# Performance work log

Hardware: AMD Instinct MI355X
Metric: run time of the kernel (lower is better)

The kernel has to match this reference:

```python
import jax, jax.numpy as jnp
import numpy as np

B, N, D = 32, 2048, 16
PCD = 2        # point_cloud_dimensions
K_NN = 16      # k nearest neighbours
FILTERS = 64


def setup_inputs() -> dict:
    key = jax.random.key(0)
    k1, k2, k3 = jax.random.split(key, 3)
    x = jax.random.normal(k1, (B, N, D), dtype=jnp.float32)
    # 1x1 Conv2D == dense over the last (channel) dim: W [D, FILTERS], b [FILTERS]
    W = jax.random.normal(k2, (D, FILTERS), dtype=jnp.float32) * (1.0 / np.sqrt(D))
    b = jnp.zeros((FILTERS,), dtype=jnp.float32)
    return {"x": x, "W": W, "b": b}


def reference(x, W, b):
    # points = first PCD channels; features = full input (dynamic_coordinates=True)
    points = x[:, :, :PCD]                                   # [B,N,PCD]
    # squared pairwise distances: ||p_i||^2 + ||p_j||^2 - 2 p_i.p_j  -> [B,N,N]
    sq = jnp.sum(points * points, axis=-1)                   # [B,N]
    dist = sq[:, :, None] + sq[:, None, :] - 2.0 * jnp.einsum(
        'bnd,bmd->bnm', points, points)
    # k nearest neighbours (smallest distance) per point -> [B,N,k]
    _, idx = jax.lax.top_k(-dist, K_NN)
    # gather neighbour features: [B,N,k,D]
    neigh = jax.vmap(lambda f, i: f[i])(x, idx)
    centre = x[:, :, None, :]                                # [B,N,1,D]
    # NOTE: source concatenates along the neighbour axis -> [B,N,k+1,D]
    edges = jnp.concatenate([centre, neigh - centre], axis=2)
    # 1x1 conv (linear activation) over channel dim: [B,N,k+1,FILTERS]
    conv = jnp.einsum('bnkd,df->bnkf', edges, W) + b
    # Max pooling over neighbour axis: [B,N,FILTERS]
    pooled = jnp.max(conv, axis=2)
    # shortcut_input_features=True: concat original features
    return jnp.concatenate([pooled, x], axis=-1)             # [B,N,FILTERS+D]
```

## Files before the change

### kernel.cpp

```cpp
#include <hip/hip_runtime.h>


#define B_  32
#define N_  2048
#define D_  16
#define F_  64
#define K_  16
#define OUTD (F_ + D_)
#define NQ  64
#define NS  4
#define SPLIT (N_ / NS)
#define CAP 24

typedef _Float16 h2 __attribute__((ext_vector_type(2)));

static __device__ __forceinline__ h2 h2min(h2 a, h2 b) { return __builtin_elementwise_min(a, b); }
static __device__ __forceinline__ h2 h2max(h2 a, h2 b) { return __builtin_elementwise_max(a, b); }
static __device__ __forceinline__ _Float16 hmn(_Float16 a, _Float16 b) { return __builtin_elementwise_min(a, b); }
static __device__ __forceinline__ _Float16 hmx(_Float16 a, _Float16 b) { return __builtin_elementwise_max(a, b); }
static __device__ __forceinline__ unsigned short h2b(_Float16 h) { return __builtin_bit_cast(unsigned short, h); }
static __device__ __forceinline__ _Float16 b2h(unsigned short b) { return __builtin_bit_cast(_Float16, b); }

static __device__ __forceinline__ void pair_ins(_Float16 (&k)[16], _Float16 y0, _Float16 y1) {
#pragma unroll
    for (int j = 15; j >= 2; --j)
        k[j] = hmn(hmn(k[j], hmx(k[j - 1], y0)), hmx(k[j - 2], y1));
    k[1] = hmn(hmn(k[1], hmx(k[0], y0)), y1);
    k[0] = hmn(k[0], y0);
}

static __device__ __forceinline__ float vdist(float2 qp, float sqn, float2 p, float sm) {
    float dot = __fmaf_rn(qp.y, p.y, __fmul_rn(qp.x, p.x));
    return __fsub_rn(__fadd_rn(sqn, sm), __fmul_rn(2.f, dot));
}

__global__ __launch_bounds__(256) void proj_kernel(const float* __restrict__ x,
                                                   const float* __restrict__ W,
                                                   float* __restrict__ Y) {
    __shared__ float Ws[D_ * F_];
    __shared__ float xs[16][D_];
    const int t = threadIdx.x;
    for (int i = t; i < D_ * F_; i += 256) Ws[i] = W[i];
    const int p0 = blockIdx.x * 16;
    ((float*)xs)[t] = x[(size_t)p0 * D_ + t];
    __syncthreads();
    const int w = t >> 6, f = t & 63;
#pragma unroll
    for (int i = 0; i < 4; i++) {
        const int pw = w * 4 + i;
        float acc = 0.f;
#pragma unroll
        for (int d = 0; d < D_; d++) acc = fmaf(xs[pw][d], Ws[d * F_ + f], acc);
        Y[(size_t)(p0 + pw) * F_ + f] = acc;
    }
}

__global__ __launch_bounds__(256, 4) void knn_kernel(const float* __restrict__ x,
                                                     const float* __restrict__ bias,
                                                     const float* __restrict__ Y,
                                                     float* __restrict__ out) {
    __shared__ float2 pts[N_];
    __shared__ float  sqs[N_];
    __shared__ __align__(16) char region[NS * NQ * CAP * 2];
    __shared__ unsigned short idxL[NQ][18];
    __shared__ int   scnt[NS][NQ];
    __shared__ float TubA[NQ];

    unsigned (*arr32)[NQ][9] = (unsigned (*)[NQ][9])region;
    unsigned short (*survb)[NQ][CAP] = (unsigned short (*)[NQ][CAP])region;

    const int b = blockIdx.x >> 5;
    const int qbase = (blockIdx.x & 31) * NQ;
    const int t = threadIdx.x;
    const int s = t >> 6;
    const int qi = t & 63;
    const int q = qbase + qi;

    const float* xb = x + (size_t)b * N_ * D_;
    for (int m = t; m < N_; m += 256) {
        float2 p = make_float2(xb[m * D_ + 0], xb[m * D_ + 1]);
        pts[m] = p;
        sqs[m] = __fadd_rn(__fmul_rn(p.x, p.x), __fmul_rn(p.y, p.y));
    }
    __syncthreads();

    const float2 qp = pts[q];
    const float sqn = sqs[q];
    const float n2x = -2.0f * qp.x, n2y = -2.0f * qp.y;

    h2 key2[16];
    const _Float16 hinf = b2h((unsigned short)0x7C00);
#pragma unroll
    for (int j = 0; j < 16; ++j) key2[j] = (h2){hinf, hinf};

    const int m0 = s * SPLIT, m1 = m0 + SPLIT;
#pragma unroll 4
    for (int m = m0; m < m1; m += 2) {
        float2 pa = pts[m];     float sa = sqs[m];
        float2 pb = pts[m + 1]; float sb = sqs[m + 1];
        float da = __fmaf_rn(n2y, pa.y, __fmaf_rn(n2x, pa.x, sqn + sa));
        float db = __fmaf_rn(n2y, pb.y, __fmaf_rn(n2x, pb.x, sqn + sb));
        h2 v = __builtin_bit_cast(h2, __builtin_amdgcn_cvt_pkrtz(da, db));
#pragma unroll
        for (int j = 15; j >= 1; --j)
            key2[j] = h2min(key2[j], h2max(key2[j - 1], v));
        key2[0] = h2min(key2[0], v);
    }

    _Float16 keyl[16];
#pragma unroll
    for (int j = 0; j < 16; ++j) keyl[j] = key2[j].x;
#pragma unroll
    for (int tt = 0; tt < 8; ++tt) pair_ins(keyl, key2[2 * tt].y, key2[2 * tt + 1].y);

    if (s > 0) {
#pragma unroll
        for (int tt = 0; tt < 8; ++tt)
            arr32[s - 1][qi][tt] =
                (unsigned)h2b(keyl[2 * tt]) | ((unsigned)h2b(keyl[2 * tt + 1]) << 16);
    }
    __syncthreads();

    if (s == 0) {
        for (int ss = 0; ss < NS - 1; ++ss) {
#pragma unroll
            for (int tt = 0; tt < 8; ++tt) {
                unsigned w32 = arr32[ss][qi][tt];
                pair_ins(keyl, b2h((unsigned short)(w32 & 0xffffu)),
                               b2h((unsigned short)(w32 >> 16)));
            }
        }
        float tub = (float)b2h((unsigned short)(h2b(keyl[15]) + 2));
        TubA[qi] = fmaxf(tub, 7e-5f);
    }
    __syncthreads();

    const float Tub = TubA[qi];
    int sc = 0;
#pragma unroll 2
    for (int m = m0; m < m1; ++m) {
        float d = vdist(qp, sqn, pts[m], sqs[m]);
        if (d < Tub) { if (sc < CAP) survb[s][qi][sc] = (unsigned short)m; sc++; }
    }
    scnt[s][qi] = sc;
    __syncthreads();

    if (s == 0) {
        float key[16];
#pragma unroll
        for (int j = 0; j < 16; ++j) key[j] = INFINITY;
        for (int ss = 0; ss < NS; ++ss) {
            int n = scnt[ss][qi]; n = n < CAP ? n : CAP;
            for (int j = 0; j < n; ++j) {
                int m = (int)survb[ss][qi][j];
                float d = vdist(qp, sqn, pts[m], sqs[m]);
#pragma unroll
                for (int jj = 15; jj >= 1; --jj)
                    key[jj] = fminf(key[jj], fmaxf(key[jj - 1], d));
                key[0] = fminf(key[0], d);
            }
        }
        const float T = key[15];
        int w = 0;
        for (int ss = 0; ss < NS; ++ss) {
            int n = scnt[ss][qi]; n = n < CAP ? n : CAP;
            for (int j = 0; j < n; ++j) {
                int m = (int)survb[ss][qi][j];
                float d = vdist(qp, sqn, pts[m], sqs[m]);
                if (d < T && w < K_) idxL[qi][w++] = (unsigned short)m;
            }
        }
        for (int ss = 0; ss < NS && w < K_; ++ss) {
            int n = scnt[ss][qi]; n = n < CAP ? n : CAP;
            for (int j = 0; j < n && w < K_; ++j) {
                int m = (int)survb[ss][qi][j];
                float d = vdist(qp, sqn, pts[m], sqs[m]);
                if (d == T) idxL[qi][w++] = (unsigned short)m;
            }
        }
    }
    __syncthreads();

    const int f = qi;
    const float bf = bias[f];
    const float* Yb = Y + (size_t)b * N_ * F_;
    for (int i = 0; i < 16; i++) {
        const int qq = s * 16 + i;
        const int gq = qbase + qq;
        const float yn = Yb[(size_t)gq * F_ + f];
        float M = -INFINITY;
#pragma unroll
        for (int k = 0; k < K_; k++) {
            int m = (int)idxL[qq][k];
            M = fmaxf(M, Yb[(size_t)m * F_ + f]);
        }
        const size_t pb = (size_t)b * N_ + gq;
        out[pb * OUTD + f] = fmaxf(yn, M - yn) + bf;
        if (f < D_) out[pb * OUTD + F_ + f] = xb[(size_t)gq * D_ + f];
    }
}

extern "C" void kernel_launch(void* const* d_in, const int* in_sizes, int n_in,
                              void* d_out, int out_size, void* d_ws, size_t ws_size,
                              hipStream_t stream) {
    const float* x    = (const float*)d_in[0];
    const float* W    = (const float*)d_in[1];
    const float* bias = (const float*)d_in[2];
    float* out = (float*)d_out;

    float* Y = (float*)d_ws;

    proj_kernel<<<B_ * N_ / 16, 256, 0, stream>>>(x, W, Y);
    knn_kernel <<<B_ * (N_ / NQ), 256, 0, stream>>>(x, bias, Y, out);
}
```

Baseline: 251.9 us.

## Process 128 queries per 512-thread kNN block to amortize point staging

Each kNN block now handles 128 queries with 512 threads (two groups of four split waves) instead of 64 queries with 256 threads. This halves the number of blocks that load the batch's 2048 points and squared norms into shared memory, so that staging cost is shared across more queries. It also clamps the survivor count when it is stored and pads any unfilled neighbour slots with the query itself, guarding against uninitialized indices. The larger block uses more shared memory and threads, which may lower occupancy, and the grid shrinks to 512 blocks.

New measurement: 259.8 us. +3.1%, slower.

```diff
diff --git a/kernel.cpp b/kernel.cpp
--- a/kernel.cpp
+++ b/kernel.cpp
@@ -7,7 +7,7 @@
 #define F_  64
 #define K_  16
 #define OUTD (F_ + D_)
-#define NQ  64
+#define NQB 128
 #define NS  4
 #define SPLIT (N_ / NS)
 #define CAP 24
@@ -27,11 +27,6 @@
         k[j] = hmn(hmn(k[j], hmx(k[j - 1], y0)), hmx(k[j - 2], y1));
     k[1] = hmn(hmn(k[1], hmx(k[0], y0)), y1);
     k[0] = hmn(k[0], y0);
-}
-
-static __device__ __forceinline__ float vdist(float2 qp, float sqn, float2 p, float sm) {
-    float dot = __fmaf_rn(qp.y, p.y, __fmul_rn(qp.x, p.x));
-    return __fsub_rn(__fadd_rn(sqn, sm), __fmul_rn(2.f, dot));
 }
 
 __global__ __launch_bounds__(256) void proj_kernel(const float* __restrict__ x,
@@ -55,29 +50,32 @@
     }
 }
 
-__global__ __launch_bounds__(256, 4) void knn_kernel(const float* __restrict__ x,
+__global__ __launch_bounds__(512, 2) void knn_kernel(const float* __restrict__ x,
                                                      const float* __restrict__ bias,
                                                      const float* __restrict__ Y,
                                                      float* __restrict__ out) {
     __shared__ float2 pts[N_];
     __shared__ float  sqs[N_];
-    __shared__ __align__(16) char region[NS * NQ * CAP * 2];
-    __shared__ unsigned short idxL[NQ][18];
-    __shared__ int   scnt[NS][NQ];
-    __shared__ float TubA[NQ];
-
-    unsigned (*arr32)[NQ][9] = (unsigned (*)[NQ][9])region;
-    unsigned short (*survb)[NQ][CAP] = (unsigned short (*)[NQ][CAP])region;
-
-    const int b = blockIdx.x >> 5;
-    const int qbase = (blockIdx.x & 31) * NQ;
+    __shared__ __align__(16) char region[NS * NQB * CAP * 2];
+    __shared__ unsigned short idxL[NQB][18];
+    __shared__ int   scnt[NS][NQB];
+    __shared__ float TubA[NQB];
+
+    unsigned (*arr32)[NQB][9] = (unsigned (*)[NQB][9])region;
+    unsigned short (*survb)[NQB][CAP] = (unsigned short (*)[NQB][CAP])region;
+
+    const int b = blockIdx.x >> 4;
+    const int qbase = (blockIdx.x & 15) * NQB;
     const int t = threadIdx.x;
-    const int s = t >> 6;
+    const int w8 = t >> 6;
+    const int s  = w8 & 3;
+    const int sg = w8 >> 2;
     const int qi = t & 63;
-    const int q = qbase + qi;
+    const int qloc = sg * 64 + qi;
+    const int q = qbase + qloc;
 
     const float* xb = x + (size_t)b * N_ * D_;
-    for (int m = t; m < N_; m += 256) {
+    for (int m = t; m < N_; m += 512) {
         float2 p = make_float2(xb[m * D_ + 0], xb[m * D_ + 1]);
         pts[m] = p;
         sqs[m] = __fadd_rn(__fmul_rn(p.x, p.x), __fmul_rn(p.y, p.y));
@@ -116,7 +114,7 @@
     if (s > 0) {
 #pragma unroll
         for (int tt = 0; tt < 8; ++tt)
-            arr32[s - 1][qi][tt] =
+            arr32[s - 1][qloc][tt] =
                 (unsigned)h2b(keyl[2 * tt]) | ((unsigned)h2b(keyl[2 * tt + 1]) << 16);
     }
     __syncthreads();
@@ -125,24 +123,26 @@
         for (int ss = 0; ss < NS - 1; ++ss) {
 #pragma unroll
             for (int tt = 0; tt < 8; ++tt) {
-                unsigned w32 = arr32[ss][qi][tt];
+                unsigned w32 = arr32[ss][qloc][tt];
                 pair_ins(keyl, b2h((unsigned short)(w32 & 0xffffu)),
                                b2h((unsigned short)(w32 >> 16)));
             }
         }
         float tub = (float)b2h((unsigned short)(h2b(keyl[15]) + 2));
-        TubA[qi] = fmaxf(tub, 7e-5f);
-    }
-    __syncthreads();
-
-    const float Tub = TubA[qi];
+        TubA[qloc] = fmaxf(tub, 7e-5f);
+    }
+    __syncthreads();
+
+    const float Tub = TubA[qloc];
     int sc = 0;
 #pragma unroll 2
     for (int m = m0; m < m1; ++m) {
-        float d = vdist(qp, sqn, pts[m], sqs[m]);
-        if (d < Tub) { if (sc < CAP) survb[s][qi][sc] = (unsigned short)m; sc++; }
-    }
-    scnt[s][qi] = sc;
+        float2 p = pts[m];
+        float dot = __fmaf_rn(qp.y, p.y, __fmul_rn(qp.x, p.x));
+        float d   = __fsub_rn(__fadd_rn(sqn, sqs[m]), __fmul_rn(2.f, dot));
+        if (d < Tub) { if (sc < CAP) survb[s][qloc][sc] = (unsigned short)m; sc++; }
+    }
+    scnt[s][qloc] = (sc < CAP) ? sc : CAP;
     __syncthreads();
 
     if (s == 0) {
@@ -150,10 +150,12 @@
 #pragma unroll
         for (int j = 0; j < 16; ++j) key[j] = INFINITY;
         for (int ss = 0; ss < NS; ++ss) {
-            int n = scnt[ss][qi]; n = n < CAP ? n : CAP;
+            int n = scnt[ss][qloc];
             for (int j = 0; j < n; ++j) {
-                int m = (int)survb[ss][qi][j];
-                float d = vdist(qp, sqn, pts[m], sqs[m]);
+                int m = (int)survb[ss][qloc][j];
+                float2 p = pts[m];
+                float dot = __fmaf_rn(qp.y, p.y, __fmul_rn(qp.x, p.x));
+                float d   = __fsub_rn(__fadd_rn(sqn, sqs[m]), __fmul_rn(2.f, dot));
 #pragma unroll
                 for (int jj = 15; jj >= 1; --jj)
                     key[jj] = fminf(key[jj], fmaxf(key[jj - 1], d));
@@ -163,21 +165,26 @@
         const float T = key[15];
         int w = 0;
         for (int ss = 0; ss < NS; ++ss) {
-            int n = scnt[ss][qi]; n = n < CAP ? n : CAP;
+            int n = scnt[ss][qloc];
             for (int j = 0; j < n; ++j) {
-                int m = (int)survb[ss][qi][j];
-                float d = vdist(qp, sqn, pts[m], sqs[m]);
-                if (d < T && w < K_) idxL[qi][w++] = (unsigned short)m;
+                int m = (int)survb[ss][qloc][j];
+                float2 p = pts[m];
+                float dot = __fmaf_rn(qp.y, p.y, __fmul_rn(qp.x, p.x));
+                float d   = __fsub_rn(__fadd_rn(sqn, sqs[m]), __fmul_rn(2.f, dot));
+                if (d < T && w < K_) idxL[qloc][w++] = (unsigned short)m;
             }
         }
         for (int ss = 0; ss < NS && w < K_; ++ss) {
-            int n = scnt[ss][qi]; n = n < CAP ? n : CAP;
+            int n = scnt[ss][qloc];
             for (int j = 0; j < n && w < K_; ++j) {
-                int m = (int)survb[ss][qi][j];
-                float d = vdist(qp, sqn, pts[m], sqs[m]);
-                if (d == T) idxL[qi][w++] = (unsigned short)m;
-            }
-        }
+                int m = (int)survb[ss][qloc][j];
+                float2 p = pts[m];
+                float dot = __fmaf_rn(qp.y, p.y, __fmul_rn(qp.x, p.x));
+                float d   = __fsub_rn(__fadd_rn(sqn, sqs[m]), __fmul_rn(2.f, dot));
+                if (d == T) idxL[qloc][w++] = (unsigned short)m;
+            }
+        }
+        while (w < K_) idxL[qloc][w++] = (unsigned short)q;
     }
     __syncthreads();
 
@@ -185,7 +192,7 @@
     const float bf = bias[f];
     const float* Yb = Y + (size_t)b * N_ * F_;
     for (int i = 0; i < 16; i++) {
-        const int qq = s * 16 + i;
+        const int qq = w8 * 16 + i;
         const int gq = qbase + qq;
         const float yn = Yb[(size_t)gq * F_ + f];
         float M = -INFINITY;
@@ -211,5 +218,5 @@
     float* Y = (float*)d_ws;
 
     proj_kernel<<<B_ * N_ / 16, 256, 0, stream>>>(x, W, Y);
-    knn_kernel <<<B_ * (N_ / NQ), 256, 0, stream>>>(x, bias, Y, out);
-}
+    knn_kernel <<<B_ * (N_ / NQB), 512, 0, stream>>>(x, bias, Y, out);
+}
```

## Bucket-sort points by x and restrict kNN scan to spatial window

Applied to the files above, without the earlier changes.

Points in each batch are counting-sorted into 64 x-buckets in shared memory, and each block processes 64 queries that are contiguous in sorted order. A first fp16 top-k pass runs over a local window of sorted neighbours to get a distance bound. That bound is used to compute an x-range, and only the buckets inside it are rescanned, so the full O(N) scan per query becomes roughly a windowed scan. This adds sort overhead, extra syncs and lower occupancy (launch bounds 3), and tie-breaking is rewritten to pick the smallest original index.

Result: slower. 384.8 us (+52.8%).

```diff
diff --git a/kernel.cpp b/kernel.cpp
--- a/kernel.cpp
+++ b/kernel.cpp
@@ -9,8 +9,8 @@
 #define OUTD (F_ + D_)
 #define NQ  64
 #define NS  4
-#define SPLIT (N_ / NS)
 #define CAP 24
+#define NB  64
 
 typedef _Float16 h2 __attribute__((ext_vector_type(2)));
 
@@ -29,9 +29,8 @@
     k[0] = hmn(k[0], y0);
 }
 
-static __device__ __forceinline__ float vdist(float2 qp, float sqn, float2 p, float sm) {
-    float dot = __fmaf_rn(qp.y, p.y, __fmul_rn(qp.x, p.x));
-    return __fsub_rn(__fadd_rn(sqn, sm), __fmul_rn(2.f, dot));
+static __device__ __forceinline__ int xbucket(float xv) {
+    return (int)fminf(fmaxf((xv + 5.0f) * 6.4f, 0.0f), 63.0f);
 }
 
 __global__ __launch_bounds__(256) void proj_kernel(const float* __restrict__ x,
@@ -55,17 +54,21 @@
     }
 }
 
-__global__ __launch_bounds__(256, 4) void knn_kernel(const float* __restrict__ x,
+__global__ __launch_bounds__(256, 3) void knn_kernel(const float* __restrict__ x,
                                                      const float* __restrict__ bias,
                                                      const float* __restrict__ Y,
                                                      float* __restrict__ out) {
-    __shared__ float2 pts[N_];
-    __shared__ float  sqs[N_];
-    __shared__ __align__(16) char region[NS * NQ * CAP * 2];
+    __shared__ float2 sxy[N_];
+    __shared__ float  ssq[N_];
+    __shared__ unsigned short sidx[N_];
+    __shared__ __align__(16) char region[16384];
+    __shared__ unsigned int   bstart[NB + 1];
+    __shared__ unsigned int   bcnt[NB];
+    __shared__ float TubA[NQ];
     __shared__ unsigned short idxL[NQ][18];
-    __shared__ int   scnt[NS][NQ];
-    __shared__ float TubA[NQ];
-
+    __shared__ unsigned short scnt[NS][NQ];
+
+    unsigned char (*tab)[NB] = (unsigned char (*)[NB])region;
     unsigned (*arr32)[NQ][9] = (unsigned (*)[NQ][9])region;
     unsigned short (*survb)[NQ][CAP] = (unsigned short (*)[NQ][CAP])region;
 
@@ -74,75 +77,142 @@
     const int t = threadIdx.x;
     const int s = t >> 6;
     const int qi = t & 63;
-    const int q = qbase + qi;
 
     const float* xb = x + (size_t)b * N_ * D_;
-    for (int m = t; m < N_; m += 256) {
-        float2 p = make_float2(xb[m * D_ + 0], xb[m * D_ + 1]);
-        pts[m] = p;
-        sqs[m] = __fadd_rn(__fmul_rn(p.x, p.x), __fmul_rn(p.y, p.y));
-    }
-    __syncthreads();
-
-    const float2 qp = pts[q];
-    const float sqn = sqs[q];
+    float2 p8[8];
+    int bk8[8];
+#pragma unroll
+    for (int j = 0; j < 8; ++j) {
+        const int m = t * 8 + j;
+        p8[j] = make_float2(xb[m * D_ + 0], xb[m * D_ + 1]);
+        bk8[j] = xbucket(p8[j].x);
+    }
+    for (int i = t; i < 4096; i += 256) ((unsigned*)region)[i] = 0u;
+    __syncthreads();
+
+#pragma unroll
+    for (int j = 0; j < 8; ++j) tab[t][bk8[j]]++;
+    __syncthreads();
+
+    if (t < NB) {
+        unsigned run = 0;
+        for (int i = 0; i < 256; ++i) {
+            unsigned c = tab[i][t];
+            tab[i][t] = (unsigned char)run;
+            run += c;
+        }
+        bcnt[t] = run;
+    }
+    __syncthreads();
+
+    if (t == 0) {
+        unsigned acc = 0;
+        for (int i = 0; i < NB; ++i) { bstart[i] = acc; acc += bcnt[i]; }
+        bstart[NB] = acc;
+    }
+    __syncthreads();
+
+#pragma unroll
+    for (int j = 0; j < 8; ++j) {
+        const int bk = bk8[j];
+        int loc = 0;
+#pragma unroll
+        for (int jj = 0; jj < 8; ++jj) if (jj < j && bk8[jj] == bk) loc++;
+        const int sr = (int)bstart[bk] + (int)tab[t][bk] + loc;
+        const float2 p = p8[j];
+        sxy[sr] = p;
+        ssq[sr] = __fadd_rn(__fmul_rn(p.x, p.x), __fmul_rn(p.y, p.y));
+        sidx[sr] = (unsigned short)(t * 8 + j);
+    }
+    __syncthreads();
+
+    const int qrank = qbase + qi;
+    const float2 qp = sxy[qrank];
+    const float sqn = ssq[qrank];
+    const int   mq  = (int)sidx[qrank];
     const float n2x = -2.0f * qp.x, n2y = -2.0f * qp.y;
 
+    const _Float16 hinf = b2h((unsigned short)0x7C00);
     h2 key2[16];
-    const _Float16 hinf = b2h((unsigned short)0x7C00);
-#pragma unroll
-    for (int j = 0; j < 16; ++j) key2[j] = (h2){hinf, hinf};
-
-    const int m0 = s * SPLIT, m1 = m0 + SPLIT;
-#pragma unroll 4
-    for (int m = m0; m < m1; m += 2) {
-        float2 pa = pts[m];     float sa = sqs[m];
-        float2 pb = pts[m + 1]; float sb = sqs[m + 1];
-        float da = __fmaf_rn(n2y, pa.y, __fmaf_rn(n2x, pa.x, sqn + sa));
-        float db = __fmaf_rn(n2y, pb.y, __fmaf_rn(n2x, pb.x, sqn + sb));
-        h2 v = __builtin_bit_cast(h2, __builtin_amdgcn_cvt_pkrtz(da, db));
-#pragma unroll
-        for (int j = 15; j >= 1; --j)
-            key2[j] = h2min(key2[j], h2max(key2[j - 1], v));
-        key2[0] = h2min(key2[0], v);
-    }
-
     _Float16 keyl[16];
-#pragma unroll
-    for (int j = 0; j < 16; ++j) keyl[j] = key2[j].x;
-#pragma unroll
-    for (int tt = 0; tt < 8; ++tt) pair_ins(keyl, key2[2 * tt].y, key2[2 * tt + 1].y);
-
-    if (s > 0) {
-#pragma unroll
-        for (int tt = 0; tt < 8; ++tt)
-            arr32[s - 1][qi][tt] =
-                (unsigned)h2b(keyl[2 * tt]) | ((unsigned)h2b(keyl[2 * tt + 1]) << 16);
-    }
-    __syncthreads();
-
-    if (s == 0) {
-        for (int ss = 0; ss < NS - 1; ++ss) {
-#pragma unroll
-            for (int tt = 0; tt < 8; ++tt) {
-                unsigned w32 = arr32[ss][qi][tt];
-                pair_ins(keyl, b2h((unsigned short)(w32 & 0xffffu)),
-                               b2h((unsigned short)(w32 >> 16)));
-            }
-        }
-        float tub = (float)b2h((unsigned short)(h2b(keyl[15]) + 2));
-        TubA[qi] = fmaxf(tub, 7e-5f);
-    }
-    __syncthreads();
-
+
+#define SCAN(LOV, HIV)                                                          \
+    {                                                                           \
+        _Pragma("unroll") for (int j = 0; j < 16; ++j) key2[j] = (h2){hinf, hinf}; \
+        const int Lsc = (HIV) - (LOV);                                          \
+        const int Lq = (((Lsc + 3) >> 2) + 1) & ~1;                             \
+        const int p0 = (LOV) + s * Lq;                                          \
+        for (int i = 0; i < Lq; i += 2) {                                       \
+            int p = p0 + i;                                                     \
+            int pc = (p > N_ - 2) ? (N_ - 2) : p;                               \
+            float2 pa = sxy[pc];     float sa = ssq[pc];                        \
+            float2 pb = sxy[pc + 1]; float sb = ssq[pc + 1];                    \
+            float da = __fmaf_rn(n2y, pa.y, __fmaf_rn(n2x, pa.x, sqn + sa));    \
+            float db = __fmaf_rn(n2y, pb.y, __fmaf_rn(n2x, pb.x, sqn + sb));    \
+            if (p != pc || p >= (HIV)) da = INFINITY;                           \
+            if (p + 1 >= (HIV)) db = INFINITY;                                  \
+            h2 v = __builtin_bit_cast(h2, __builtin_amdgcn_cvt_pkrtz(da, db));  \
+            _Pragma("unroll") for (int j = 15; j >= 1; --j)                     \
+                key2[j] = h2min(key2[j], h2max(key2[j - 1], v));                \
+            key2[0] = h2min(key2[0], v);                                        \
+        }                                                                       \
+        _Pragma("unroll") for (int j = 0; j < 16; ++j) keyl[j] = key2[j].x;     \
+        _Pragma("unroll") for (int tt = 0; tt < 8; ++tt)                        \
+            pair_ins(keyl, key2[2 * tt].y, key2[2 * tt + 1].y);                 \
+        if (s > 0) {                                                            \
+            _Pragma("unroll") for (int tt = 0; tt < 8; ++tt)                    \
+                arr32[s - 1][qi][tt] = (unsigned)h2b(keyl[2 * tt]) |            \
+                                       ((unsigned)h2b(keyl[2 * tt + 1]) << 16); \
+        }                                                                       \
+        __syncthreads();                                                        \
+        if (s == 0) {                                                           \
+            for (int ss = 0; ss < NS - 1; ++ss) {                               \
+                _Pragma("unroll") for (int tt = 0; tt < 8; ++tt) {              \
+                    unsigned w32 = arr32[ss][qi][tt];                           \
+                    pair_ins(keyl, b2h((unsigned short)(w32 & 0xffffu)),        \
+                                   b2h((unsigned short)(w32 >> 16)));           \
+                }                                                               \
+            }                                                                   \
+            float tub = (float)b2h((unsigned short)(h2b(keyl[15]) + 2));        \
+            TubA[qi] = fmaxf(tub, 7e-5f);                                       \
+        }                                                                       \
+        __syncthreads();                                                        \
+    }
+
+    const int winLo = (qbase - 80 > 0) ? (qbase - 80) : 0;
+    const int winHi = (qbase + NQ + 80 < N_) ? (qbase + NQ + 80) : N_;
+    SCAN(winLo, winHi)
+    const float T0 = TubA[qi];
+
+    const float r = sqrtf(T0 * 1.005f) * 1.0001f + 1e-6f;
+    float xLo = qp.x - r, xHi = qp.x + r;
+    for (int off = 32; off; off >>= 1) {
+        xLo = fminf(xLo, __shfl_xor(xLo, off));
+        xHi = fmaxf(xHi, __shfl_xor(xHi, off));
+    }
+    int Lo2 = (int)bstart[xbucket(xLo)];
+    int Hi2 = (int)bstart[xbucket(xHi) + 1];
+    if (winLo < Lo2) Lo2 = winLo;
+    if (winHi > Hi2) Hi2 = winHi;
+
+    SCAN(Lo2, Hi2)
     const float Tub = TubA[qi];
-    int sc = 0;
-#pragma unroll 2
-    for (int m = m0; m < m1; ++m) {
-        float d = vdist(qp, sqn, pts[m], sqs[m]);
-        if (d < Tub) { if (sc < CAP) survb[s][qi][sc] = (unsigned short)m; sc++; }
-    }
-    scnt[s][qi] = sc;
+
+    {
+        const int Lsc = Hi2 - Lo2;
+        const int Lq = (((Lsc + 3) >> 2) + 1) & ~1;
+        const int p0 = Lo2 + s * Lq;
+        int sc = 0;
+        for (int i = 0; i < Lq; ++i) {
+            int p = p0 + i;
+            if (p >= Hi2) break;
+            float2 pp = sxy[p];
+            float dot = __fmaf_rn(qp.y, pp.y, __fmul_rn(qp.x, pp.x));
+            float d   = __fsub_rn(__fadd_rn(sqn, ssq[p]), __fmul_rn(2.f, dot));
+            if (d < Tub) { if (sc < CAP) survb[s][qi][sc] = (unsigned short)p; sc++; }
+        }
+        scnt[s][qi] = (unsigned short)((sc < CAP) ? sc : CAP);
+    }
     __syncthreads();
 
     if (s == 0) {
@@ -150,10 +220,12 @@
 #pragma unroll
         for (int j = 0; j < 16; ++j) key[j] = INFINITY;
         for (int ss = 0; ss < NS; ++ss) {
-            int n = scnt[ss][qi]; n = n < CAP ? n : CAP;
+            int n = (int)scnt[ss][qi];
             for (int j = 0; j < n; ++j) {
-                int m = (int)survb[ss][qi][j];
-                float d = vdist(qp, sqn, pts[m], sqs[m]);
+                int rr = (int)survb[ss][qi][j];
+                float2 pp = sxy[rr];
+                float dot = __fmaf_rn(qp.y, pp.y, __fmul_rn(qp.x, pp.x));
+                float d   = __fsub_rn(__fadd_rn(sqn, ssq[rr]), __fmul_rn(2.f, dot));
 #pragma unroll
                 for (int jj = 15; jj >= 1; --jj)
                     key[jj] = fminf(key[jj], fmaxf(key[jj - 1], d));
@@ -163,21 +235,36 @@
         const float T = key[15];
         int w = 0;
         for (int ss = 0; ss < NS; ++ss) {
-            int n = scnt[ss][qi]; n = n < CAP ? n : CAP;
+            int n = (int)scnt[ss][qi];
             for (int j = 0; j < n; ++j) {
-                int m = (int)survb[ss][qi][j];
-                float d = vdist(qp, sqn, pts[m], sqs[m]);
-                if (d < T && w < K_) idxL[qi][w++] = (unsigned short)m;
+                int rr = (int)survb[ss][qi][j];
+                float2 pp = sxy[rr];
+                float dot = __fmaf_rn(qp.y, pp.y, __fmul_rn(qp.x, pp.x));
+                float d   = __fsub_rn(__fadd_rn(sqn, ssq[rr]), __fmul_rn(2.f, dot));
+                if (d < T && w < K_) idxL[qi][w++] = sidx[rr];
             }
         }
-        for (int ss = 0; ss < NS && w < K_; ++ss) {
-            int n = scnt[ss][qi]; n = n < CAP ? n : CAP;
-            for (int j = 0; j < n && w < K_; ++j) {
-                int m = (int)survb[ss][qi][j];
-                float d = vdist(qp, sqn, pts[m], sqs[m]);
-                if (d == T) idxL[qi][w++] = (unsigned short)m;
+        int last = -1;
+        while (w < K_) {
+            int best = 70000;
+            for (int ss = 0; ss < NS; ++ss) {
+                int n = (int)scnt[ss][qi];
+                for (int j = 0; j < n; ++j) {
+                    int rr = (int)survb[ss][qi][j];
+                    float2 pp = sxy[rr];
+                    float dot = __fmaf_rn(qp.y, pp.y, __fmul_rn(qp.x, pp.x));
+                    float d   = __fsub_rn(__fadd_rn(sqn, ssq[rr]), __fmul_rn(2.f, dot));
+                    if (d == T) {
+                        int o = (int)sidx[rr];
+                        if (o > last && o < best) best = o;
+                    }
+                }
             }
-        }
+            if (best == 70000) break;
+            idxL[qi][w++] = (unsigned short)best;
+            last = best;
+        }
+        while (w < K_) idxL[qi][w++] = (unsigned short)mq;
     }
     __syncthreads();
 
@@ -186,17 +273,17 @@
     const float* Yb = Y + (size_t)b * N_ * F_;
     for (int i = 0; i < 16; i++) {
         const int qq = s * 16 + i;
-        const int gq = qbase + qq;
-        const float yn = Yb[(size_t)gq * F_ + f];
+        const int go = (int)sidx[qbase + qq];
+        const float yn = Yb[(size_t)go * F_ + f];
         float M = -INFINITY;
 #pragma unroll
         for (int k = 0; k < K_; k++) {
             int m = (int)idxL[qq][k];
             M = fmaxf(M, Yb[(size_t)m * F_ + f]);
         }
-        const size_t pb = (size_t)b * N_ + gq;
+        const size_t pb = (size_t)b * N_ + go;
         out[pb * OUTD + f] = fmaxf(yn, M - yn) + bf;
-        if (f < D_) out[pb * OUTD + F_ + f] = xb[(size_t)gq * D_ + f];
+        if (f < D_) out[pb * OUTD + F_ + f] = xb[(size_t)go * D_ + f];
     }
 }
 
```
